# Kernel tuning notes

Measured on AMD Instinct MI355X. Metric: run time of the kernel, lower is better.

## Reference

```python
import jax, jax.numpy as jnp
import numpy as np

N_NODES = 50000
N_EDGES = 800000
D_IN = 128
D_HID = 128
D_OUT = 128


def gcn_conv(x, W, b, src, dst, n_nodes):
    """PyG GCNConv: sym-normalized A+I aggregation, then bias.
    messages flow src -> dst; self-loops handled analytically."""
    h = x @ W  # [N, F_out]
    ones = jnp.ones(src.shape[0], dtype=h.dtype)
    deg = jax.ops.segment_sum(ones, dst, num_segments=n_nodes) + 1.0  # +1 self-loop
    dinv = jax.lax.rsqrt(deg)  # deg^-1/2
    norm = dinv[src] * dinv[dst]  # [E]
    agg = jax.ops.segment_sum(h[src] * norm[:, None], dst, num_segments=n_nodes)
    out = agg + h * (dinv * dinv)[:, None]  # self-loop term: dinv[i]^2 * h[i]
    return out + b


def setup_inputs() -> dict:
    key = jax.random.key(0)
    ks = jax.random.split(key, 12)
    x = jax.random.normal(ks[0], (N_NODES, D_IN), dtype=jnp.float32)
    edge_index = jax.random.randint(ks[1], (2, N_EDGES), 0, N_NODES, dtype=jnp.int64)

    def lin(k, fi, fo):
        s = 1.0 / np.sqrt(fi)
        return jax.random.uniform(k, (fi, fo), jnp.float32, -s, s)

    return {
        "x": x,
        "edge_index": edge_index,
        "W1": lin(ks[2], D_IN, D_HID), "b1": jnp.zeros((D_HID,), jnp.float32),
        "W2": lin(ks[3], D_HID, D_HID), "b2": jnp.zeros((D_HID,), jnp.float32),
        "W3": lin(ks[4], D_HID, D_OUT), "b3": jnp.zeros((D_OUT,), jnp.float32),
        "Wm1": lin(ks[5], 2 * D_HID, D_HID), "bm1": jnp.zeros((D_HID,), jnp.float32),
        "Wm2": lin(ks[6], D_HID, D_HID), "bm2": jnp.zeros((D_HID,), jnp.float32),
    }


def reference(x, edge_index, W1, b1, W2, b2, W3, b3, Wm1, bm1, Wm2, bm2):
    src, dst = edge_index[0], edge_index[1]
    n = x.shape[0]
    h = jax.nn.relu(gcn_conv(x, W1, b1, src, dst, n))
    h = jax.nn.relu(gcn_conv(h, W2, b2, src, dst, n))
    h = gcn_conv(h, W3, b3, src, dst, n)
    # edge head: gather node pairs, concat, 2-layer MLP
    ef = jnp.concatenate([h[src], h[dst]], axis=1)  # [E, 2*hidden]
    es = jax.nn.relu(ef @ Wm1 + bm1) @ Wm2 + bm2  # [E, hidden]
    return jnp.squeeze(es)
```

## Files before the change

kernel.cpp:

```cpp
#include <hip/hip_runtime.h>
#include <stdint.h>

typedef __attribute__((ext_vector_type(8))) short bf16x8;
typedef __attribute__((ext_vector_type(4))) float f32x4;

static __device__ __forceinline__ unsigned short f2b(float f) {
    unsigned int u = __float_as_uint(f);
    unsigned int r = u + 0x7fffu + ((u >> 16) & 1u);
    return (unsigned short)(r >> 16);
}
static __device__ __forceinline__ float b2f(unsigned short u) {
    return __uint_as_float((unsigned int)u << 16);
}
static __device__ __forceinline__ f32x4 b2f4(ushort4 u) {
    f32x4 r;
    r[0] = b2f(u.x); r[1] = b2f(u.y); r[2] = b2f(u.z); r[3] = b2f(u.w);
    return r;
}


__global__ __launch_bounds__(256) void count_and_gemm1(
        const int* __restrict__ dst, int E, int* __restrict__ counts, int ecnt,
        const float* __restrict__ x, const float* __restrict__ W1,
        unsigned short* __restrict__ outb, int N) {
    __shared__ __align__(16) unsigned short hl[64][136];
    int tid = threadIdx.x;
    if ((int)blockIdx.x < ecnt) {
        int e = blockIdx.x * 256 + tid;
        if (e < E) atomicAdd(&counts[dst[e]], 1);
        return;
    }
    int tilebase = (blockIdx.x - ecnt) * 64;
    int wid = tid >> 6, lane = tid & 63;
    int lg = lane >> 4, l15 = lane & 15;

    bf16x8 a[2][4];
    #pragma unroll
    for (int mt = 0; mt < 2; ++mt) {
        int col = wid * 32 + mt * 16 + l15;
        #pragma unroll
        for (int kk = 0; kk < 4; ++kk) {
            bf16x8 af;
            #pragma unroll
            for (int ee = 0; ee < 8; ++ee)
                af[ee] = (short)f2b(W1[(size_t)(kk * 32 + lg * 8 + ee) * 128 + col]);
            a[mt][kk] = af;
        }
    }
    #pragma unroll
    for (int p = 0; p < 4; ++p) {
        int idx = p * 256 + tid;
        int r = idx >> 4, ci = idx & 15;
        int row = tilebase + r;
        if (row >= N) row = N - 1;
        const float* ip = x + (size_t)row * 128 + ci * 8;
        f32x4 x0 = *(const f32x4*)ip;
        f32x4 x1 = *(const f32x4*)(ip + 4);
        uint4 v;
        v.x = (unsigned int)f2b(x0[0]) | ((unsigned int)f2b(x0[1]) << 16);
        v.y = (unsigned int)f2b(x0[2]) | ((unsigned int)f2b(x0[3]) << 16);
        v.z = (unsigned int)f2b(x1[0]) | ((unsigned int)f2b(x1[1]) << 16);
        v.w = (unsigned int)f2b(x1[2]) | ((unsigned int)f2b(x1[3]) << 16);
        *(uint4*)&hl[r][ci * 8] = v;
    }
    __syncthreads();

    f32x4 acc[2][4];
    #pragma unroll
    for (int mt = 0; mt < 2; ++mt)
        #pragma unroll
        for (int nt = 0; nt < 4; ++nt) acc[mt][nt] = (f32x4){0.f, 0.f, 0.f, 0.f};
    #pragma unroll
    for (int kk = 0; kk < 4; ++kk) {
        #pragma unroll
        for (int nt = 0; nt < 4; ++nt) {
            bf16x8 b = *(const bf16x8*)&hl[nt * 16 + l15][kk * 32 + lg * 8];
            acc[0][nt] = __builtin_amdgcn_mfma_f32_16x16x32_bf16(a[0][kk], b, acc[0][nt], 0, 0, 0);
            acc[1][nt] = __builtin_amdgcn_mfma_f32_16x16x32_bf16(a[1][kk], b, acc[1][nt], 0, 0, 0);
        }
    }
    #pragma unroll
    for (int mt = 0; mt < 2; ++mt) {
        int j = wid * 32 + mt * 16 + lg * 4;
        #pragma unroll
        for (int nt = 0; nt < 4; ++nt) {
            int node = tilebase + nt * 16 + l15;
            if (node < N) {
                unsigned int u0 = (unsigned int)f2b(acc[mt][nt][0]) | ((unsigned int)f2b(acc[mt][nt][1]) << 16);
                unsigned int u1 = (unsigned int)f2b(acc[mt][nt][2]) | ((unsigned int)f2b(acc[mt][nt][3]) << 16);
                *(uint2*)(outb + (size_t)node * 128 + j) = make_uint2(u0, u1);
            }
        }
    }
}


__global__ void scan_s1(const int* __restrict__ counts, int N,
                        int* __restrict__ rowstart, float* __restrict__ dinv,
                        int* __restrict__ psum) {
    __shared__ int wsum[16];
    int tid = threadIdx.x, wave = tid >> 6, lane = tid & 63;
    int i = blockIdx.x * 1024 + tid;
    int c = (i < N) ? counts[i] : 0;
    int x = c;
    #pragma unroll
    for (int off = 1; off < 64; off <<= 1) {
        int v = __shfl_up(x, off);
        if (lane >= off) x += v;
    }
    if (lane == 63) wsum[wave] = x;
    __syncthreads();
    int pre = 0, tot = 0;
    #pragma unroll
    for (int w = 0; w < 16; ++w) {
        int s = wsum[w];
        tot += s;
        if (w < wave) pre += s;
    }
    if (i < N) {
        rowstart[i] = pre + x - c;
        dinv[i] = rsqrtf((float)c + 1.0f);
    }
    if (tid == 0) psum[blockIdx.x] = tot;
}

__global__ void scan_s23(const int* __restrict__ psum, int nchunk,
                         int* __restrict__ rowstart, int N, int* __restrict__ cursor) {
    int b = blockIdx.x;
    int pre = 0, tot = 0;
    for (int w = 0; w < nchunk; ++w) {
        int s = psum[w];
        tot += s;
        if (w < b) pre += s;
    }
    int i = b * 1024 + threadIdx.x;
    if (i < N) {
        int r = rowstart[i] + pre;
        rowstart[i] = r;
        cursor[i] = r;
    }
    if (b == 0 && threadIdx.x == 0) rowstart[N] = tot;
}

__global__ void fill_csr(const int* __restrict__ src, const int* __restrict__ dst, int E,
                         int* __restrict__ cursor, const float* __restrict__ dinv,
                         int2* __restrict__ csr_sn, int* __restrict__ csr_dst,
                         int* __restrict__ csr_eid) {
    int e = blockIdx.x * 256 + threadIdx.x;
    if (e < E) {
        int d = dst[e], s = src[e];
        int p = atomicAdd(&cursor[d], 1);
        float nrm = dinv[s] * dinv[d];
        csr_sn[p] = make_int2(s, __float_as_int(nrm));
        csr_dst[p] = d;
        csr_eid[p] = e;
    }
}


__global__ __launch_bounds__(256) void node_mfma(const unsigned short* __restrict__ inp,
                                                 const float* __restrict__ W,
                                                 unsigned short* __restrict__ outb, int N) {
    __shared__ __align__(16) unsigned short hl[64][136];
    int tid = threadIdx.x;
    int wid = tid >> 6, lane = tid & 63;
    int lg = lane >> 4, l15 = lane & 15;
    int tilebase = blockIdx.x * 64;

    bf16x8 a[2][4];
    #pragma unroll
    for (int mt = 0; mt < 2; ++mt) {
        int col = wid * 32 + mt * 16 + l15;
        #pragma unroll
        for (int kk = 0; kk < 4; ++kk) {
            bf16x8 af;
            #pragma unroll
            for (int ee = 0; ee < 8; ++ee)
                af[ee] = (short)f2b(W[(size_t)(kk * 32 + lg * 8 + ee) * 128 + col]);
            a[mt][kk] = af;
        }
    }
    #pragma unroll
    for (int p = 0; p < 4; ++p) {
        int idx = p * 256 + tid;
        int r = idx >> 4, ci = idx & 15;
        int row = tilebase + r;
        if (row >= N) row = N - 1;
        *(uint4*)&hl[r][ci * 8] = *(const uint4*)(inp + (size_t)row * 128 + ci * 8);
    }
    __syncthreads();

    f32x4 acc[2][4];
    #pragma unroll
    for (int mt = 0; mt < 2; ++mt)
        #pragma unroll
        for (int nt = 0; nt < 4; ++nt) acc[mt][nt] = (f32x4){0.f, 0.f, 0.f, 0.f};
    #pragma unroll
    for (int kk = 0; kk < 4; ++kk) {
        #pragma unroll
        for (int nt = 0; nt < 4; ++nt) {
            bf16x8 b = *(const bf16x8*)&hl[nt * 16 + l15][kk * 32 + lg * 8];
            acc[0][nt] = __builtin_amdgcn_mfma_f32_16x16x32_bf16(a[0][kk], b, acc[0][nt], 0, 0, 0);
            acc[1][nt] = __builtin_amdgcn_mfma_f32_16x16x32_bf16(a[1][kk], b, acc[1][nt], 0, 0, 0);
        }
    }
    #pragma unroll
    for (int mt = 0; mt < 2; ++mt) {
        int j = wid * 32 + mt * 16 + lg * 4;
        #pragma unroll
        for (int nt = 0; nt < 4; ++nt) {
            int node = tilebase + nt * 16 + l15;
            if (node < N) {
                unsigned int u0 = (unsigned int)f2b(acc[mt][nt][0]) | ((unsigned int)f2b(acc[mt][nt][1]) << 16);
                unsigned int u1 = (unsigned int)f2b(acc[mt][nt][2]) | ((unsigned int)f2b(acc[mt][nt][3]) << 16);
                *(uint2*)(outb + (size_t)node * 128 + j) = make_uint2(u0, u1);
            }
        }
    }
}


template <int RELU>
__global__ __launch_bounds__(256) void aggregate_half(
        const unsigned short* __restrict__ tb, const int* __restrict__ rowstart,
        const int2* __restrict__ csr_sn, const float* __restrict__ dinv,
        const float* __restrict__ bias, unsigned short* __restrict__ hb,
        int N, int colbase) {
    int tid = threadIdx.x;
    int node = blockIdx.x * 16 + (tid >> 4);
    if (node >= N) return;
    int c = colbase + (tid & 15) * 4;
    float di = dinv[node];
    f32x4 self = b2f4(*(const ushort4*)(tb + (size_t)node * 128 + c));
    f32x4 acc = *(const f32x4*)(bias + c) + (di * di) * self;
    int e = rowstart[node], re = rowstart[node + 1];
    for (; e + 7 < re; e += 8) {
        int2 p0 = csr_sn[e + 0], p1 = csr_sn[e + 1], p2 = csr_sn[e + 2], p3 = csr_sn[e + 3];
        int2 p4 = csr_sn[e + 4], p5 = csr_sn[e + 5], p6 = csr_sn[e + 6], p7 = csr_sn[e + 7];
        ushort4 r0 = *(const ushort4*)(tb + (size_t)p0.x * 128 + c);
        ushort4 r1 = *(const ushort4*)(tb + (size_t)p1.x * 128 + c);
        ushort4 r2 = *(const ushort4*)(tb + (size_t)p2.x * 128 + c);
        ushort4 r3 = *(const ushort4*)(tb + (size_t)p3.x * 128 + c);
        ushort4 r4 = *(const ushort4*)(tb + (size_t)p4.x * 128 + c);
        ushort4 r5 = *(const ushort4*)(tb + (size_t)p5.x * 128 + c);
        ushort4 r6 = *(const ushort4*)(tb + (size_t)p6.x * 128 + c);
        ushort4 r7 = *(const ushort4*)(tb + (size_t)p7.x * 128 + c);
        acc += __int_as_float(p0.y) * b2f4(r0);
        acc += __int_as_float(p1.y) * b2f4(r1);
        acc += __int_as_float(p2.y) * b2f4(r2);
        acc += __int_as_float(p3.y) * b2f4(r3);
        acc += __int_as_float(p4.y) * b2f4(r4);
        acc += __int_as_float(p5.y) * b2f4(r5);
        acc += __int_as_float(p6.y) * b2f4(r6);
        acc += __int_as_float(p7.y) * b2f4(r7);
    }
    for (; e + 3 < re; e += 4) {
        int2 p0 = csr_sn[e + 0], p1 = csr_sn[e + 1], p2 = csr_sn[e + 2], p3 = csr_sn[e + 3];
        ushort4 r0 = *(const ushort4*)(tb + (size_t)p0.x * 128 + c);
        ushort4 r1 = *(const ushort4*)(tb + (size_t)p1.x * 128 + c);
        ushort4 r2 = *(const ushort4*)(tb + (size_t)p2.x * 128 + c);
        ushort4 r3 = *(const ushort4*)(tb + (size_t)p3.x * 128 + c);
        acc += __int_as_float(p0.y) * b2f4(r0);
        acc += __int_as_float(p1.y) * b2f4(r1);
        acc += __int_as_float(p2.y) * b2f4(r2);
        acc += __int_as_float(p3.y) * b2f4(r3);
    }
    for (; e < re; ++e) {
        int2 p0 = csr_sn[e];
        acc += __int_as_float(p0.y) * b2f4(*(const ushort4*)(tb + (size_t)p0.x * 128 + c));
    }
    if (RELU) {
        #pragma unroll
        for (int j = 0; j < 4; ++j) acc[j] = fmaxf(acc[j], 0.f);
    }
    unsigned int u0 = (unsigned int)f2b(acc[0]) | ((unsigned int)f2b(acc[1]) << 16);
    unsigned int u1 = (unsigned int)f2b(acc[2]) | ((unsigned int)f2b(acc[3]) << 16);
    *(uint2*)(hb + (size_t)node * 128 + c) = make_uint2(u0, u1);
}


__global__ __launch_bounds__(256) void uv_gemm(const unsigned short* __restrict__ h3b,
                                               const float* __restrict__ Wm1,
                                               unsigned short* __restrict__ uvb, int N) {
    __shared__ __align__(16) unsigned short hl[64][136];
    int tid = threadIdx.x;
    int wid = tid >> 6, lane = tid & 63;
    int lg = lane >> 4, l15 = lane & 15;
    int tilebase = blockIdx.x * 64;

    bf16x8 a[4][4];
    #pragma unroll
    for (int mt = 0; mt < 4; ++mt) {
        int jc = wid * 64 + mt * 16 + l15;
        int koff = (jc >> 7) * 128;
        int col = jc & 127;
        #pragma unroll
        for (int kk = 0; kk < 4; ++kk) {
            bf16x8 af;
            #pragma unroll
            for (int ee = 0; ee < 8; ++ee)
                af[ee] = (short)f2b(Wm1[(size_t)(koff + kk * 32 + lg * 8 + ee) * 128 + col]);
            a[mt][kk] = af;
        }
    }

    #pragma unroll
    for (int p = 0; p < 4; ++p) {
        int idx = p * 256 + tid;
        int r = idx >> 4, ci = idx & 15;
        int row = tilebase + r;
        if (row >= N) row = N - 1;
        uint4 v = *(const uint4*)(h3b + (size_t)row * 128 + ci * 8);
        *(uint4*)&hl[r][ci * 8] = v;
    }
    __syncthreads();

    f32x4 acc[4][4];
    #pragma unroll
    for (int mt = 0; mt < 4; ++mt)
        #pragma unroll
        for (int nt = 0; nt < 4; ++nt) acc[mt][nt] = (f32x4){0.f, 0.f, 0.f, 0.f};
    #pragma unroll
    for (int kk = 0; kk < 4; ++kk) {
        #pragma unroll
        for (int nt = 0; nt < 4; ++nt) {
            bf16x8 b = *(const bf16x8*)&hl[nt * 16 + l15][kk * 32 + lg * 8];
            #pragma unroll
            for (int mt = 0; mt < 4; ++mt)
                acc[mt][nt] = __builtin_amdgcn_mfma_f32_16x16x32_bf16(a[mt][kk], b, acc[mt][nt], 0, 0, 0);
        }
    }
    #pragma unroll
    for (int mt = 0; mt < 4; ++mt) {
        int jc = wid * 64 + mt * 16 + lg * 4;
        #pragma unroll
        for (int nt = 0; nt < 4; ++nt) {
            int node = tilebase + nt * 16 + l15;
            if (node < N) {
                unsigned int u0 = (unsigned int)f2b(acc[mt][nt][0]) | ((unsigned int)f2b(acc[mt][nt][1]) << 16);
                unsigned int u1 = (unsigned int)f2b(acc[mt][nt][2]) | ((unsigned int)f2b(acc[mt][nt][3]) << 16);
                *(uint2*)(uvb + (size_t)node * 256 + jc) = make_uint2(u0, u1);
            }
        }
    }
}


__global__ __launch_bounds__(256, 3) void edge_head4(
        const unsigned short* __restrict__ uvb, const int2* __restrict__ csr_sn,
        const int* __restrict__ csr_dst, const int* __restrict__ csr_eid,
        const float* __restrict__ bm1, const float* __restrict__ Wm2,
        const float* __restrict__ bm2, float* __restrict__ out, int E, int ntiles) {
    __shared__ __align__(16) unsigned short zl[64][136];
    __shared__ int eid_l[64];
    int tid = threadIdx.x;
    int wid = tid >> 6, lane = tid & 63;
    int lg = lane >> 4, l15 = lane & 15;
    int es = tid >> 4;
    int ci = tid & 15;
    int c0 = ci * 8;

    bf16x8 a2[2][4];
    float b2v[2][4];
    #pragma unroll
    for (int mt = 0; mt < 2; ++mt) {
        int m = wid * 32 + mt * 16 + l15;
        #pragma unroll
        for (int kk = 0; kk < 4; ++kk) {
            bf16x8 af;
            #pragma unroll
            for (int ee = 0; ee < 8; ++ee)
                af[ee] = (short)f2b(Wm2[(size_t)(kk * 32 + lg * 8 + ee) * 128 + m]);
            a2[mt][kk] = af;
        }
        #pragma unroll
        for (int r = 0; r < 4; ++r)
            b2v[mt][r] = bm2[wid * 32 + mt * 16 + lg * 4 + r];
    }
    float bm1v[8];
    #pragma unroll
    for (int j = 0; j < 8; ++j) bm1v[j] = bm1[c0 + j];

    uint4 uuA[4], uuB[4];
    int dA[4], dB[4], eidA[4], eidB[4];

    auto stage = [&](int tile, uint4 (&uu)[4], int (&dd)[4], int (&ee)[4]) {
        #pragma unroll
        for (int p = 0; p < 4; ++p) {
            int slot = tile * 64 + p * 16 + es;
            int cs = (slot < E) ? slot : (E - 1);
            int s = csr_sn[cs].x;
            dd[p] = csr_dst[cs];
            ee[p] = (slot < E) ? csr_eid[cs] : -1;
            uu[p] = *(const uint4*)(uvb + (size_t)s * 256 + c0);
        }
    };

    int t = blockIdx.x;
    if (t < ntiles) stage(t, uuA, dA, eidA);
    for (; t < ntiles; t += gridDim.x) {
        __syncthreads();
        #pragma unroll
        for (int p = 0; p < 4; ++p) {
            uint4 vv = *(const uint4*)(uvb + (size_t)dA[p] * 256 + 128 + c0);
            uint4 uu = uuA[p];
            float z0 = fmaxf(b2f((unsigned short)(uu.x)) + b2f((unsigned short)(vv.x)) + bm1v[0], 0.f);
            float z1 = fmaxf(b2f((unsigned short)(uu.x >> 16)) + b2f((unsigned short)(vv.x >> 16)) + bm1v[1], 0.f);
            float z2 = fmaxf(b2f((unsigned short)(uu.y)) + b2f((unsigned short)(vv.y)) + bm1v[2], 0.f);
            float z3 = fmaxf(b2f((unsigned short)(uu.y >> 16)) + b2f((unsigned short)(vv.y >> 16)) + bm1v[3], 0.f);
            float z4 = fmaxf(b2f((unsigned short)(uu.z)) + b2f((unsigned short)(vv.z)) + bm1v[4], 0.f);
            float z5 = fmaxf(b2f((unsigned short)(uu.z >> 16)) + b2f((unsigned short)(vv.z >> 16)) + bm1v[5], 0.f);
            float z6 = fmaxf(b2f((unsigned short)(uu.w)) + b2f((unsigned short)(vv.w)) + bm1v[6], 0.f);
            float z7 = fmaxf(b2f((unsigned short)(uu.w >> 16)) + b2f((unsigned short)(vv.w >> 16)) + bm1v[7], 0.f);
            uint4 w;
            w.x = (unsigned int)f2b(z0) | ((unsigned int)f2b(z1) << 16);
            w.y = (unsigned int)f2b(z2) | ((unsigned int)f2b(z3) << 16);
            w.z = (unsigned int)f2b(z4) | ((unsigned int)f2b(z5) << 16);
            w.w = (unsigned int)f2b(z6) | ((unsigned int)f2b(z7) << 16);
            *(uint4*)&zl[p * 16 + es][c0] = w;
            if (ci == 0) eid_l[p * 16 + es] = eidA[p];
        }
        int tn = t + gridDim.x;
        bool more = (tn < ntiles);
        if (more) stage(tn, uuB, dB, eidB);
        __syncthreads();

        f32x4 c2[2][4];
        #pragma unroll
        for (int mt = 0; mt < 2; ++mt)
            #pragma unroll
            for (int nt = 0; nt < 4; ++nt) c2[mt][nt] = (f32x4){0.f, 0.f, 0.f, 0.f};
        #pragma unroll
        for (int kk = 0; kk < 4; ++kk) {
            #pragma unroll
            for (int nt = 0; nt < 4; ++nt) {
                bf16x8 b = *(const bf16x8*)&zl[nt * 16 + l15][kk * 32 + lg * 8];
                c2[0][nt] = __builtin_amdgcn_mfma_f32_16x16x32_bf16(a2[0][kk], b, c2[0][nt], 0, 0, 0);
                c2[1][nt] = __builtin_amdgcn_mfma_f32_16x16x32_bf16(a2[1][kk], b, c2[1][nt], 0, 0, 0);
            }
        }
        #pragma unroll
        for (int mt = 0; mt < 2; ++mt) {
            #pragma unroll
            for (int nt = 0; nt < 4; ++nt) {
                int eg = eid_l[nt * 16 + l15];
                if (eg >= 0) {
                    f32x4 o;
                    #pragma unroll
                    for (int r = 0; r < 4; ++r) o[r] = c2[mt][nt][r] + b2v[mt][r];
                    *(f32x4*)(out + (size_t)eg * 128 + wid * 32 + mt * 16 + lg * 4) = o;
                }
            }
        }
        if (more) {
            #pragma unroll
            for (int p = 0; p < 4; ++p) {
                uuA[p] = uuB[p]; dA[p] = dB[p]; eidA[p] = eidB[p];
            }
        }
    }
}


extern "C" void kernel_launch(void* const* d_in, const int* in_sizes, int n_in,
                              void* d_out, int out_size, void* d_ws, size_t ws_size,
                              hipStream_t stream) {
    const float* x  = (const float*)d_in[0];
    const int*   ei = (const int*)d_in[1];
    const float* W1 = (const float*)d_in[2];
    const float* b1 = (const float*)d_in[3];
    const float* W2 = (const float*)d_in[4];
    const float* b2 = (const float*)d_in[5];
    const float* W3 = (const float*)d_in[6];
    const float* b3 = (const float*)d_in[7];
    const float* Wm1 = (const float*)d_in[8];
    const float* bm1 = (const float*)d_in[9];
    const float* Wm2 = (const float*)d_in[10];
    const float* bm2 = (const float*)d_in[11];
    float* out = (float*)d_out;

    const int N = in_sizes[0] / 128;
    const int E = in_sizes[1] / 2;
    const int* src = ei;
    const int* dstp = ei + E;

    uintptr_t base = (uintptr_t)d_ws;
    auto alloc = [&](size_t bytes) -> void* {
        uintptr_t p = base;
        base += (bytes + 255) & ~(uintptr_t)255;
        return (void*)p;
    };
    int*   counts   = (int*)alloc((size_t)(N + 1) * 4);
    int*   rowstart = (int*)alloc((size_t)(N + 1) * 4);
    int*   cursor   = (int*)alloc((size_t)N * 4);
    float* dinv     = (float*)alloc((size_t)N * 4);
    int*   psum     = (int*)alloc(4096);
    int2*  csr_sn   = (int2*)alloc((size_t)E * 8);
    int*   csr_d    = (int*)alloc((size_t)E * 4);
    int*   csr_e    = (int*)alloc((size_t)E * 4);
    unsigned short* tb  = (unsigned short*)alloc((size_t)N * 128 * 2);
    unsigned short* hb  = (unsigned short*)alloc((size_t)N * 128 * 2);
    unsigned short* uvb = (unsigned short*)alloc((size_t)N * 256 * 2);
    (void)ws_size; (void)n_in; (void)out_size;

    hipMemsetAsync(counts, 0, (size_t)(N + 1) * 4, stream);

    int egrid = (E + 255) / 256;
    int nchunk = (N + 1023) / 1024;
    int ggrid = (N + 63) / 64;
    int sgrid = (N + 15) / 16;

    count_and_gemm1<<<egrid + ggrid, 256, 0, stream>>>(dstp, E, counts, egrid, x, W1, tb, N);
    scan_s1<<<nchunk, 1024, 0, stream>>>(counts, N, rowstart, dinv, psum);
    scan_s23<<<nchunk, 1024, 0, stream>>>(psum, nchunk, rowstart, N, cursor);
    fill_csr<<<egrid, 256, 0, stream>>>(src, dstp, E, cursor, dinv, csr_sn, csr_d, csr_e);

    aggregate_half<1><<<sgrid, 256, 0, stream>>>(tb, rowstart, csr_sn, dinv, b1, hb, N, 0);
    aggregate_half<1><<<sgrid, 256, 0, stream>>>(tb, rowstart, csr_sn, dinv, b1, hb, N, 64);
    node_mfma<<<ggrid, 256, 0, stream>>>(hb, W2, tb, N);
    aggregate_half<1><<<sgrid, 256, 0, stream>>>(tb, rowstart, csr_sn, dinv, b2, hb, N, 0);
    aggregate_half<1><<<sgrid, 256, 0, stream>>>(tb, rowstart, csr_sn, dinv, b2, hb, N, 64);
    node_mfma<<<ggrid, 256, 0, stream>>>(hb, W3, tb, N);
    aggregate_half<0><<<sgrid, 256, 0, stream>>>(tb, rowstart, csr_sn, dinv, b3, hb, N, 0);
    aggregate_half<0><<<sgrid, 256, 0, stream>>>(tb, rowstart, csr_sn, dinv, b3, hb, N, 64);

    uv_gemm<<<ggrid, 256, 0, stream>>>(hb, Wm1, uvb, N);

    int ntiles = (E + 63) / 64;
    int hgrid = ntiles < 768 ? ntiles : 768;
    edge_head4<<<hgrid, 256, 0, stream>>>(uvb, csr_sn, csr_d, csr_e, bm1, Wm2, bm2, out, E, ntiles);
}
```

Measured before the change: 443.4 us.

## Sort CSR rows by edge id, merge aggregate halves, pack edge metadata

Adds a rank_csr pass that orders each destination's edges by original edge id, so the CSR layout no longer depends on atomic ordering. It also writes a packed int4 (src, dst, eid, norm) array that the edge head reads with a single load. The two half-column aggregate launches per layer are merged into one kernel covering all 128 columns with 32 threads per node, which halves the CSR traversal. The cost is an extra O(deg^2) ranking kernel plus extra memory writes.

```diff
diff --git a/kernel.cpp b/kernel.cpp
--- a/kernel.cpp
+++ b/kernel.cpp
@@ -157,6 +157,21 @@
     }
 }
 
+__global__ void rank_csr(const int* __restrict__ rowstart, const int* __restrict__ csr_dst,
+                         const int2* __restrict__ csr_sn, const int* __restrict__ csr_eid,
+                         int2* __restrict__ csr_sn2, int4* __restrict__ csr_sde, int E) {
+    int p = blockIdx.x * 256 + threadIdx.x;
+    if (p >= E) return;
+    int d = csr_dst[p];
+    int rs = rowstart[d], re = rowstart[d + 1];
+    int my = csr_eid[p];
+    int rank = 0;
+    for (int q = rs; q < re; ++q) rank += (csr_eid[q] < my);
+    int2 sn = csr_sn[p];
+    csr_sn2[rs + rank] = sn;
+    csr_sde[rs + rank] = make_int4(sn.x, d, my, sn.y);
+}
+
 
 __global__ __launch_bounds__(256) void node_mfma(const unsigned short* __restrict__ inp,
                                                  const float* __restrict__ W,
@@ -221,15 +236,14 @@
 
 
 template <int RELU>
-__global__ __launch_bounds__(256) void aggregate_half(
+__global__ __launch_bounds__(256) void aggregate(
         const unsigned short* __restrict__ tb, const int* __restrict__ rowstart,
         const int2* __restrict__ csr_sn, const float* __restrict__ dinv,
-        const float* __restrict__ bias, unsigned short* __restrict__ hb,
-        int N, int colbase) {
+        const float* __restrict__ bias, unsigned short* __restrict__ hb, int N) {
     int tid = threadIdx.x;
-    int node = blockIdx.x * 16 + (tid >> 4);
+    int node = blockIdx.x * 8 + (tid >> 5);
     if (node >= N) return;
-    int c = colbase + (tid & 15) * 4;
+    int c = (tid & 31) * 4;
     float di = dinv[node];
     f32x4 self = b2f4(*(const ushort4*)(tb + (size_t)node * 128 + c));
     f32x4 acc = *(const f32x4*)(bias + c) + (di * di) * self;
@@ -347,8 +361,7 @@
 
 
 __global__ __launch_bounds__(256, 3) void edge_head4(
-        const unsigned short* __restrict__ uvb, const int2* __restrict__ csr_sn,
-        const int* __restrict__ csr_dst, const int* __restrict__ csr_eid,
+        const unsigned short* __restrict__ uvb, const int4* __restrict__ csr_sde,
         const float* __restrict__ bm1, const float* __restrict__ Wm2,
         const float* __restrict__ bm2, float* __restrict__ out, int E, int ntiles) {
     __shared__ __align__(16) unsigned short zl[64][136];
@@ -389,10 +402,10 @@
         for (int p = 0; p < 4; ++p) {
             int slot = tile * 64 + p * 16 + es;
             int cs = (slot < E) ? slot : (E - 1);
-            int s = csr_sn[cs].x;
-            dd[p] = csr_dst[cs];
-            ee[p] = (slot < E) ? csr_eid[cs] : -1;
-            uu[p] = *(const uint4*)(uvb + (size_t)s * 256 + c0);
+            int4 sde = csr_sde[cs];
+            dd[p] = sde.y;
+            ee[p] = (slot < E) ? sde.z : -1;
+            uu[p] = *(const uint4*)(uvb + (size_t)sde.x * 256 + c0);
         }
     };
 
@@ -498,6 +511,8 @@
     int2*  csr_sn   = (int2*)alloc((size_t)E * 8);
     int*   csr_d    = (int*)alloc((size_t)E * 4);
     int*   csr_e    = (int*)alloc((size_t)E * 4);
+    int2*  csr_sn2  = (int2*)alloc((size_t)E * 8);
+    int4*  csr_sde  = (int4*)alloc((size_t)E * 16);
     unsigned short* tb  = (unsigned short*)alloc((size_t)N * 128 * 2);
     unsigned short* hb  = (unsigned short*)alloc((size_t)N * 128 * 2);
     unsigned short* uvb = (unsigned short*)alloc((size_t)N * 256 * 2);
@@ -508,25 +523,23 @@
     int egrid = (E + 255) / 256;
     int nchunk = (N + 1023) / 1024;
     int ggrid = (N + 63) / 64;
-    int sgrid = (N + 15) / 16;
+    int agrid = (N + 7) / 8;
 
     count_and_gemm1<<<egrid + ggrid, 256, 0, stream>>>(dstp, E, counts, egrid, x, W1, tb, N);
     scan_s1<<<nchunk, 1024, 0, stream>>>(counts, N, rowstart, dinv, psum);
     scan_s23<<<nchunk, 1024, 0, stream>>>(psum, nchunk, rowstart, N, cursor);
     fill_csr<<<egrid, 256, 0, stream>>>(src, dstp, E, cursor, dinv, csr_sn, csr_d, csr_e);
-
-    aggregate_half<1><<<sgrid, 256, 0, stream>>>(tb, rowstart, csr_sn, dinv, b1, hb, N, 0);
-    aggregate_half<1><<<sgrid, 256, 0, stream>>>(tb, rowstart, csr_sn, dinv, b1, hb, N, 64);
+    rank_csr<<<egrid, 256, 0, stream>>>(rowstart, csr_d, csr_sn, csr_e, csr_sn2, csr_sde, E);
+
+    aggregate<1><<<agrid, 256, 0, stream>>>(tb, rowstart, csr_sn2, dinv, b1, hb, N);
     node_mfma<<<ggrid, 256, 0, stream>>>(hb, W2, tb, N);
-    aggregate_half<1><<<sgrid, 256, 0, stream>>>(tb, rowstart, csr_sn, dinv, b2, hb, N, 0);
-    aggregate_half<1><<<sgrid, 256, 0, stream>>>(tb, rowstart, csr_sn, dinv, b2, hb, N, 64);
+    aggregate<1><<<agrid, 256, 0, stream>>>(tb, rowstart, csr_sn2, dinv, b2, hb, N);
     node_mfma<<<ggrid, 256, 0, stream>>>(hb, W3, tb, N);
-    aggregate_half<0><<<sgrid, 256, 0, stream>>>(tb, rowstart, csr_sn, dinv, b3, hb, N, 0);
-    aggregate_half<0><<<sgrid, 256, 0, stream>>>(tb, rowstart, csr_sn, dinv, b3, hb, N, 64);
+    aggregate<0><<<agrid, 256, 0, stream>>>(tb, rowstart, csr_sn2, dinv, b3, hb, N);
 
     uv_gemm<<<ggrid, 256, 0, stream>>>(hb, Wm1, uvb, N);
 
     int ntiles = (E + 63) / 64;
     int hgrid = ntiles < 768 ? ntiles : 768;
-    edge_head4<<<hgrid, 256, 0, stream>>>(uvb, csr_sn, csr_d, csr_e, bm1, Wm2, bm2, out, E, ntiles);
-}
+    edge_head4<<<hgrid, 256, 0, stream>>>(uvb, csr_sde, bm1, Wm2, bm2, out, E, ntiles);
+}
```

After: 434.0 us. 1.02x faster.
